# Optimization experiments

Measured on AMD Instinct MI355X. Metric: run time of the kernel, lower is better.

The kernel has to match this reference:

```python
import jax, jax.numpy as jnp
import numpy as np

B, F, C, H, W = 4, 16, 768, 16, 16   # video: b f c h w
L, M = 64, 16                        # audio: b c l m
NH = 12                              # num_heads
WS_V = 4                             # local_window (video window size, frames)
GROUPS = 32                          # GroupNorm32
EPS = 1e-5


def group_norm(x, scale, bias):
    # x: [b, c, t]; normalize over (channels-within-group, t)
    b, c, t = x.shape
    xg = x.reshape(b, GROUPS, c // GROUPS, t)
    mu = xg.mean(axis=(2, 3), keepdims=True)
    var = xg.var(axis=(2, 3), keepdims=True)
    xg = (xg - mu) * jax.lax.rsqrt(var + EPS)
    return xg.reshape(b, c, t) * scale[None, :, None] + bias[None, :, None]


def setup_inputs() -> dict:
    key = jax.random.key(0)
    ks = jax.random.split(key, 8)
    s = 0.02
    return {
        "video": jax.random.normal(ks[0], (B, F, C, H, W), jnp.float32),
        "audio": jax.random.normal(ks[1], (B, C, L, M), jnp.float32),
        "vn_scale": jnp.ones((C,), jnp.float32),
        "vn_bias": jnp.zeros((C,), jnp.float32),
        "an_scale": jnp.ones((C,), jnp.float32),
        "an_bias": jnp.zeros((C,), jnp.float32),
        "vqkv_w": jax.random.normal(ks[2], (3 * C, C), jnp.float32) * s,
        "vqkv_b": jnp.zeros((3 * C,), jnp.float32),
        "aqkv_w": jax.random.normal(ks[3], (3 * C, C), jnp.float32) * s,
        "aqkv_b": jnp.zeros((3 * C,), jnp.float32),
        "vproj_w": jax.random.normal(ks[4], (C, C), jnp.float32) * s,  # zero_module in orig; random for nontrivial baseline
        "vproj_b": jnp.zeros((C,), jnp.float32),
        "aproj_w": jax.random.normal(ks[5], (C, C), jnp.float32) * s,
        "aproj_b": jnp.zeros((C,), jnp.float32),
    }


def reference(video, audio, vn_scale, vn_bias, an_scale, an_bias,
              vqkv_w, vqkv_b, aqkv_w, aqkv_b,
              vproj_w, vproj_b, aproj_w, aproj_b):
    b, f, c, h, w = video.shape
    _, _, l, m = audio.shape
    ch = c // NH
    scale = ch ** -0.25
    ws_audio = WS_V * l // f
    nwin = f // WS_V
    wsv_tok = WS_V * h * w      # video tokens per window
    wsa_tok = ws_audio * m      # audio tokens per window

    vt = jnp.transpose(video, (0, 2, 1, 3, 4)).reshape(b, c, f * h * w)  # b c (f h w)
    at = audio.reshape(b, c, l * m)                                       # b c (l m)

    # 1x1 conv qkv after GroupNorm
    vqkv = jnp.einsum('oc,bct->bot', vqkv_w, group_norm(vt, vn_scale, vn_bias)) + vqkv_b[None, :, None]
    aqkv = jnp.einsum('oc,bct->bot', aqkv_w, group_norm(at, an_scale, an_bias)) + aqkv_b[None, :, None]
    q_v, k_v, v_v = jnp.split(vqkv, 3, axis=1)
    q_a, k_a, v_a = jnp.split(aqkv, 3, axis=1)

    # attention_index with window_shift = 0
    va_index = (jnp.arange(wsa_tok)[None, :] + (jnp.arange(nwin) * wsa_tok)[:, None]) % (l * m)
    av_index = (jnp.arange(wsv_tok)[None, :] + (jnp.arange(nwin) * wsv_tok)[:, None]) % (f * h * w)

    def heads(x):
        return x.reshape(b, NH, ch, -1)

    # video queries attend gathered audio windows
    qv = heads(q_v).reshape(b, NH, ch, nwin, wsv_tok)
    ka = jnp.take(heads(k_a), va_index, axis=-1)   # [b,NH,ch,nwin,wsa_tok]
    vav = jnp.take(heads(v_a), va_index, axis=-1)
    wts = jax.nn.softmax(jnp.einsum('bhcnt,bhcns->bhnts', qv * scale, ka * scale), axis=-1)
    v_out = jnp.einsum('bhnts,bhcns->bhcnt', wts, vav).reshape(b, c, f * h * w)

    # audio queries attend gathered video windows
    qa = heads(q_a).reshape(b, NH, ch, nwin, wsa_tok)
    kv = jnp.take(heads(k_v), av_index, axis=-1)   # [b,NH,ch,nwin,wsv_tok]
    vvv = jnp.take(heads(v_v), av_index, axis=-1)
    wts = jax.nn.softmax(jnp.einsum('bhcnt,bhcns->bhnts', qa * scale, kv * scale), axis=-1)
    a_out = jnp.einsum('bhnts,bhcns->bhcnt', wts, vvv).reshape(b, c, l * m)

    # zero-init 1x1x1 / 1x1 proj_out convs + residual
    vh = jnp.transpose(v_out.reshape(b, c, f, h, w), (0, 2, 1, 3, 4))  # b f c h w
    vh = jnp.einsum('oc,bfchw->bfohw', vproj_w, vh) + vproj_b[None, None, :, None, None]
    ah = jnp.einsum('oc,bclm->bolm', aproj_w, a_out.reshape(b, c, l, m)) + aproj_b[None, :, None, None]
    return video + vh, audio + ah
```

## Files before the change

kernel.cpp:

```cpp
#include <hip/hip_runtime.h>
#include <hip/hip_bf16.h>

typedef unsigned short ushort_t;
typedef __attribute__((ext_vector_type(8))) short short8;
typedef __attribute__((ext_vector_type(4))) float f32x4;

#define DI __device__ __forceinline__

DI float b2f(unsigned int u16) {
  union { unsigned int i; float f; } v;
  v.i = u16 << 16;
  return v.f;
}
DI ushort_t f2b(float f) {
  union { float f; unsigned int u; } v; v.f = f;
  unsigned int r = v.u + 0x7FFFu + ((v.u >> 16) & 1u);
  return (ushort_t)(r >> 16);
}

DI void gl_lds16(const ushort_t* g, ushort_t* l) {
  __builtin_amdgcn_global_load_lds(
      (const __attribute__((address_space(1))) unsigned int*)g,
      (__attribute__((address_space(3))) unsigned int*)l, 16, 0, 0);
}

__global__ void wcvt_kernel(const float* __restrict__ w0, const float* __restrict__ w1,
                            const float* __restrict__ w2, const float* __restrict__ w3,
                            ushort_t* __restrict__ o0, ushort_t* __restrict__ o1,
                            ushort_t* __restrict__ o2, ushort_t* __restrict__ o3) {
  const int n1 = 2304 * 768, n3 = 768 * 768;
  const int total = 2 * n1 + 2 * n3;
  for (int i = blockIdx.x * blockDim.x + threadIdx.x; i < total; i += gridDim.x * blockDim.x) {
    if (i < n1) o0[i] = f2b(w0[i]);
    else if (i < 2 * n1) o1[i - n1] = f2b(w1[i - n1]);
    else if (i < 2 * n1 + n3) o2[i - 2 * n1] = f2b(w2[i - 2 * n1]);
    else o3[i - 2 * n1 - n3] = f2b(w3[i - 2 * n1 - n3]);
  }
}

__global__ void gn_partial_kernel(const float* __restrict__ video,
                                  const float* __restrict__ audio,
                                  float* __restrict__ part) {
  const int bid = blockIdx.x;
  const int tid = threadIdx.x;
  float s = 0.f, ss = 0.f;
  if (bid < 2048) {
    int bg = bid >> 4, f = bid & 15;
    int b = bg >> 5, g = bg & 31;
    const float* base = video + ((size_t)((b * 16 + f) * 768 + g * 24)) * 256 + tid;
#pragma unroll
    for (int cl = 0; cl < 24; ++cl) {
      float v = base[cl * 256];
      s += v; ss += v * v;
    }
  } else {
    int a = bid - 2048;
    int bg = a >> 2, p = a & 3;
    int b = bg >> 5, g = bg & 31;
    const float* base = audio + ((size_t)(b * 768 + g * 24)) * 1024 + p * 256 + tid;
#pragma unroll
    for (int cl = 0; cl < 24; ++cl) {
      float v = base[cl * 1024];
      s += v; ss += v * v;
    }
  }
  for (int off = 32; off > 0; off >>= 1) { s += __shfl_down(s, off, 64); ss += __shfl_down(ss, off, 64); }
  __shared__ float red[8];
  int wv = tid >> 6, ln = tid & 63;
  if (ln == 0) { red[wv * 2] = s; red[wv * 2 + 1] = ss; }
  __syncthreads();
  if (tid == 0) {
    part[bid * 2] = red[0] + red[2] + red[4] + red[6];
    part[bid * 2 + 1] = red[1] + red[3] + red[5] + red[7];
  }
}

__global__ void gn_final_kernel(const float* __restrict__ part,
                                float* __restrict__ mu, float* __restrict__ rs) {
  const int tid = threadIdx.x;
  float s = 0.f, ss = 0.f;
  if (tid < 128) {
#pragma unroll
    for (int i = 0; i < 16; ++i) { s += part[(tid * 16 + i) * 2]; ss += part[(tid * 16 + i) * 2 + 1]; }
    const float N = 24.f * 4096.f;
    float m = s / N;
    mu[tid] = m;
    rs[tid] = rsqrtf(ss / N - m * m + 1e-5f);
  } else {
    int a = tid - 128;
#pragma unroll
    for (int i = 0; i < 4; ++i) { s += part[(2048 + a * 4 + i) * 2]; ss += part[(2048 + a * 4 + i) * 2 + 1]; }
    const float N = 24.f * 1024.f;
    float m = s / N;
    mu[tid] = m;
    rs[tid] = rsqrtf(ss / N - m * m + 1e-5f);
  }
}

__global__ void norm_video_kernel(const float* __restrict__ video,
                                  const float* __restrict__ mu, const float* __restrict__ rs,
                                  const float* __restrict__ sc, const float* __restrict__ bi,
                                  ushort_t* __restrict__ Xv) {
  __shared__ float T[32][257];
  const int bx = blockIdx.x;
  const int bf = bx / 24, ct = bx % 24;
  const int b = bf >> 4, f = bf & 15;
  const int c0 = ct * 32;
  const int tid = threadIdx.x;
  for (int i = 0; i < 32; ++i) {
    int c = c0 + i;
    int g = c / 24;
    float m = mu[b * 32 + g], r = rs[b * 32 + g];
    float v = video[((size_t)((b * 16 + f) * 768 + c)) * 256 + tid];
    T[i][tid] = (v - m) * r * sc[c] + bi[c];
  }
  __syncthreads();
  for (int i = 0; i < 32; ++i) {
    int id = i * 256 + tid;
    int c = id & 31, hw = id >> 5;
    Xv[((size_t)(b * 4096 + f * 256 + hw)) * 768 + c0 + c] = f2b(T[c][hw]);
  }
}

__global__ void norm_audio_kernel(const float* __restrict__ audio,
                                  const float* __restrict__ mu, const float* __restrict__ rs,
                                  const float* __restrict__ sc, const float* __restrict__ bi,
                                  ushort_t* __restrict__ Xa) {
  __shared__ float T[32][257];
  const int bx = blockIdx.x;
  const int bt = bx / 24, ct = bx % 24;
  const int b = bt >> 2, t0 = (bt & 3) * 256;
  const int c0 = ct * 32;
  const int tid = threadIdx.x;
  for (int i = 0; i < 32; ++i) {
    int c = c0 + i;
    int g = c / 24;
    float m = mu[128 + b * 32 + g], r = rs[128 + b * 32 + g];
    float v = audio[((size_t)(b * 768 + c)) * 1024 + t0 + tid];
    T[i][tid] = (v - m) * r * sc[c] + bi[c];
  }
  __syncthreads();
  for (int i = 0; i < 32; ++i) {
    int id = i * 256 + tid;
    int c = id & 31, tt = id >> 5;
    Xa[((size_t)(b * 1024 + t0 + tt)) * 768 + c0 + c] = f2b(T[c][tt]);
  }
}

template <int MODE>
__global__ __launch_bounds__(256) void gemm_kernel(
    const ushort_t* __restrict__ A, const ushort_t* __restrict__ W,
    const float* __restrict__ bias,
    void* __restrict__ p0, void* __restrict__ p1, void* __restrict__ p2,
    int M) {
  __shared__ ushort_t sm[32768];
  const int tid = threadIdx.x;
  const int lane = tid & 63, wave = tid >> 6;
  const int quad = lane >> 4, l16 = lane & 15;
  const int nwg = gridDim.x * gridDim.y;
  const int orig = blockIdx.x + gridDim.x * blockIdx.y;
  const int lid = (orig & 7) * (nwg >> 3) + (orig >> 3);
  const int n0 = (lid % gridDim.x) * 128, m0 = (lid / gridDim.x) * 128;
  const int wm = (wave & 1) * 64, wn = (wave >> 1) * 64;

  const int srow = wave * 32 + (lane >> 3);
  const int sq = ((lane & 7) ^ (lane >> 3)) * 8;
  const ushort_t* gA = A + (size_t)(m0 + srow) * 768 + sq;
  const ushort_t* gB = W + (size_t)(n0 + srow) * 768 + sq;

  f32x4 acc[4][4];
#pragma unroll
  for (int i = 0; i < 4; ++i)
#pragma unroll
    for (int j = 0; j < 4; ++j) acc[i][j] = (f32x4){0.f, 0.f, 0.f, 0.f};

  auto stage = [&](int kc, int cur) {
    ushort_t* lA = sm + cur * 8192 + wave * 2048;
    ushort_t* lB = sm + 16384 + cur * 8192 + wave * 2048;
#pragma unroll
    for (int i = 0; i < 4; ++i) {
      gl_lds16(gA + (size_t)i * 8 * 768 + kc, lA + i * 512);
      gl_lds16(gB + (size_t)i * 8 * 768 + kc, lB + i * 512);
    }
  };

  stage(0, 0);
  __syncthreads();
  int cur = 0;
  for (int t = 0; t < 12; ++t) {
    if (t < 11) stage((t + 1) * 64, cur ^ 1);
    const ushort_t* cA = sm + cur * 8192;
    const ushort_t* cB = sm + 16384 + cur * 8192;
#pragma unroll
    for (int ks = 0; ks < 2; ++ks) {
      short8 av[4], bv[4];
#pragma unroll
      for (int im = 0; im < 4; ++im) {
        int rr = wm + im * 16 + l16;
        av[im] = *reinterpret_cast<const short8*>(
            cA + rr * 64 + (((ks * 4 + quad) ^ (rr & 7)) * 8));
      }
#pragma unroll
      for (int in = 0; in < 4; ++in) {
        int rr = wn + in * 16 + l16;
        bv[in] = *reinterpret_cast<const short8*>(
            cB + rr * 64 + (((ks * 4 + quad) ^ (rr & 7)) * 8));
      }
#pragma unroll
      for (int im = 0; im < 4; ++im)
#pragma unroll
        for (int in = 0; in < 4; ++in)
          acc[im][in] = __builtin_amdgcn_mfma_f32_16x16x32_bf16(av[im], bv[in], acc[im][in], 0, 0, 0);
    }
    __syncthreads();
    cur ^= 1;
  }

  ushort_t* sC = sm;
  if (MODE == 0) {
    const int section = n0 / 768;
    const int obase = n0 - section * 768;
    if (section < 2) {
#pragma unroll
      for (int in = 0; in < 4; ++in) {
        int ol = wn + in * 16 + l16;
        float bv_ = bias[n0 + ol];
#pragma unroll
        for (int im = 0; im < 4; ++im)
#pragma unroll
          for (int r = 0; r < 4; ++r) {
            int row = wm + im * 16 + quad * 4 + r;
            sC[row * 136 + ol] = f2b(acc[im][in][r] + bv_);
          }
      }
      __syncthreads();
      ushort_t* dst = (ushort_t*)(section == 0 ? p0 : p1);
#pragma unroll
      for (int i = 0; i < 8; ++i) {
        int cid = i * 256 + tid;
        int row = cid >> 4, ch = cid & 15;
        *reinterpret_cast<uint4*>(dst + (size_t)(m0 + row) * 768 + obase + ch * 8) =
            *reinterpret_cast<const uint4*>(sC + row * 136 + ch * 8);
      }
    } else {
#pragma unroll
      for (int in = 0; in < 4; ++in) {
        int ol = wn + in * 16 + l16;
        float bv_ = bias[n0 + ol];
#pragma unroll
        for (int im = 0; im < 4; ++im)
#pragma unroll
          for (int r = 0; r < 4; ++r) {
            int mr = wm + im * 16 + quad * 4 + r;
            sC[ol * 136 + mr] = f2b(acc[im][in][r] + bv_);
          }
      }
      __syncthreads();
      ushort_t* dst = (ushort_t*)p2;
#pragma unroll
      for (int i = 0; i < 8; ++i) {
        int cid = i * 256 + tid;
        int o = cid >> 4, ch = cid & 15;
        *reinterpret_cast<uint4*>(dst + (size_t)(obase + o) * M + m0 + ch * 8) =
            *reinterpret_cast<const uint4*>(sC + o * 136 + ch * 8);
      }
    }
  } else {
#pragma unroll
    for (int in = 0; in < 4; ++in) {
      int ol = wn + in * 16 + l16;
      float bv_ = bias[n0 + ol];
#pragma unroll
      for (int im = 0; im < 4; ++im)
#pragma unroll
        for (int r = 0; r < 4; ++r) {
          int mr = wm + im * 16 + quad * 4 + r;
          sC[ol * 136 + mr] = f2b(acc[im][in][r] + bv_);
        }
    }
    __syncthreads();
    float* outp = (float*)p0;
    const float* resp = (const float*)p1;
#pragma unroll
    for (int i = 0; i < 16; ++i) {
      int cid = i * 256 + tid;
      int o = cid >> 5, ch = cid & 31;
      uint2 pk = *reinterpret_cast<const uint2*>(sC + o * 136 + ch * 4);
      size_t gidx;
      if (MODE == 1) {
        int b = m0 >> 12, f = (m0 >> 8) & 15, hw0 = m0 & 255;
        gidx = ((size_t)((b * 16 + f) * 768 + n0 + o)) * 256 + hw0 + ch * 4;
      } else {
        int b = m0 >> 10, t0 = m0 & 1023;
        gidx = ((size_t)(b * 768 + n0 + o)) * 1024 + t0 + ch * 4;
      }
      float4 rv = *reinterpret_cast<const float4*>(resp + gidx);
      float4 ov;
      ov.x = rv.x + b2f(pk.x & 0xffff);
      ov.y = rv.y + b2f(pk.x >> 16);
      ov.z = rv.z + b2f(pk.y & 0xffff);
      ov.w = rv.w + b2f(pk.y >> 16);
      *reinterpret_cast<float4*>(outp + gidx) = ov;
    }
  }
}

template <int QW, int SW>
__global__ __launch_bounds__(256) void attn_mfma_kernel(
    const ushort_t* __restrict__ Qt, const ushort_t* __restrict__ Kt,
    const ushort_t* __restrict__ Vc, ushort_t* __restrict__ Ot,
    int TQb, int TSb, int Ms) {
  __shared__ ushort_t sK[128 * 72];
  __shared__ ushort_t sP[64 * 136];
  const int tid = threadIdx.x;
  const int lane = tid & 63, wave = tid >> 6;
  const int quad = lane >> 4, l16 = lane & 15;
  const int NQT = QW / 64;
  const int bx = blockIdx.x;
  const int qt = bx % NQT;
  const int win = (bx / NQT) & 3;
  const int h = (bx / (NQT * 4)) % 12;
  const int b = bx / (NQT * 48);
  const int hc = h * 64;
  const int nq0 = b * TQb + win * QW + qt * 64;
  const int ns_base = b * TSb + win * SW;

#pragma unroll
  for (int i = 0; i < 2; ++i) {
    int c = i * 256 + tid;
    int row = c >> 3, cc = c & 7;
    uint4 raw = *reinterpret_cast<const uint4*>(Qt + (size_t)(nq0 + row) * 768 + hc + cc * 8);
    unsigned int* rp = reinterpret_cast<unsigned int*>(&raw);
    uint4 out;
    unsigned int* op = reinterpret_cast<unsigned int*>(&out);
#pragma unroll
    for (int j = 0; j < 4; ++j) {
      unsigned int lo = (unsigned int)f2b(0.125f * b2f(rp[j] & 0xffff));
      unsigned int hi = (unsigned int)f2b(0.125f * b2f(rp[j] >> 16));
      op[j] = lo | (hi << 16);
    }
    *reinterpret_cast<uint4*>(sK + row * 72 + cc * 8) = out;
  }
  __syncthreads();
  short8 qf[2];
#pragma unroll
  for (int ks = 0; ks < 2; ++ks)
    qf[ks] = *reinterpret_cast<const short8*>(sK + (wave * 16 + l16) * 72 + ks * 32 + quad * 8);

  float mr[4], lr[4];
  f32x4 on[4];
#pragma unroll
  for (int r = 0; r < 4; ++r) { mr[r] = -1e30f; lr[r] = 0.f; }
#pragma unroll
  for (int nc = 0; nc < 4; ++nc) on[nc] = (f32x4){0.f, 0.f, 0.f, 0.f};

  for (int t = 0; t < SW / 128; ++t) {
    const int ns0 = ns_base + t * 128;
    __syncthreads();
#pragma unroll
    for (int i = 0; i < 4; ++i) {
      int c = i * 256 + tid;
      int row = c >> 3, cc = c & 7;
      *reinterpret_cast<uint4*>(sK + row * 72 + cc * 8) =
          *reinterpret_cast<const uint4*>(Kt + (size_t)(ns0 + row) * 768 + hc + cc * 8);
    }
    __syncthreads();
    f32x4 sf[8];
#pragma unroll
    for (int nt = 0; nt < 8; ++nt) sf[nt] = (f32x4){0.f, 0.f, 0.f, 0.f};
#pragma unroll
    for (int ks = 0; ks < 2; ++ks) {
#pragma unroll
      for (int nt = 0; nt < 8; ++nt) {
        short8 kf = *reinterpret_cast<const short8*>(sK + (nt * 16 + l16) * 72 + ks * 32 + quad * 8);
        sf[nt] = __builtin_amdgcn_mfma_f32_16x16x32_bf16(qf[ks], kf, sf[nt], 0, 0, 0);
      }
    }
#pragma unroll
    for (int r = 0; r < 4; ++r) {
      float m_ = sf[0][r];
#pragma unroll
      for (int nt = 1; nt < 8; ++nt) m_ = fmaxf(m_, sf[nt][r]);
#pragma unroll
      for (int off = 1; off < 16; off <<= 1) m_ = fmaxf(m_, __shfl_xor(m_, off));
      float mnew = fmaxf(mr[r], m_);
      float al = __expf(mr[r] - mnew);
      float ls = 0.f;
      int prow = (wave * 16 + quad * 4 + r) * 136;
#pragma unroll
      for (int nt = 0; nt < 8; ++nt) {
        float p = __expf(sf[nt][r] - mnew);
        ls += p;
        sP[prow + nt * 16 + l16] = f2b(p);
      }
#pragma unroll
      for (int off = 1; off < 16; off <<= 1) ls += __shfl_xor(ls, off);
      lr[r] = lr[r] * al + ls;
      mr[r] = mnew;
#pragma unroll
      for (int nc = 0; nc < 4; ++nc) on[nc][r] *= al;
    }
    __syncthreads();
#pragma unroll
    for (int i = 0; i < 4; ++i) {
      int c = i * 256 + tid;
      int ch = c >> 4, cc = c & 15;
      *reinterpret_cast<uint4*>(sK + ch * 136 + cc * 8) =
          *reinterpret_cast<const uint4*>(Vc + (size_t)(hc + ch) * Ms + ns0 + cc * 8);
    }
    __syncthreads();
#pragma unroll
    for (int ks = 0; ks < 4; ++ks) {
      short8 pf = *reinterpret_cast<const short8*>(sP + (wave * 16 + l16) * 136 + ks * 32 + quad * 8);
#pragma unroll
      for (int nc = 0; nc < 4; ++nc) {
        short8 vf = *reinterpret_cast<const short8*>(sK + (nc * 16 + l16) * 136 + ks * 32 + quad * 8);
        on[nc] = __builtin_amdgcn_mfma_f32_16x16x32_bf16(pf, vf, on[nc], 0, 0, 0);
      }
    }
  }
#pragma unroll
  for (int r = 0; r < 4; ++r) {
    float inv = 1.f / lr[r];
    int prow = (wave * 16 + quad * 4 + r) * 136;
#pragma unroll
    for (int nc = 0; nc < 4; ++nc)
      sP[prow + nc * 16 + l16] = f2b(on[nc][r] * inv);
  }
  __syncthreads();
#pragma unroll
  for (int i = 0; i < 2; ++i) {
    int c = i * 256 + tid;
    int row = c >> 3, cc = c & 7;
    *reinterpret_cast<uint4*>(Ot + (size_t)(nq0 + row) * 768 + hc + cc * 8) =
        *reinterpret_cast<const uint4*>(sP + row * 136 + cc * 8);
  }
}

extern "C" void kernel_launch(void* const* d_in, const int* in_sizes, int n_in,
                              void* d_out, int out_size, void* d_ws, size_t ws_size,
                              hipStream_t stream) {
  (void)in_sizes; (void)n_in; (void)out_size; (void)ws_size;
  const float* video = (const float*)d_in[0];
  const float* audio = (const float*)d_in[1];
  const float* vn_s = (const float*)d_in[2];
  const float* vn_b = (const float*)d_in[3];
  const float* an_s = (const float*)d_in[4];
  const float* an_b = (const float*)d_in[5];
  const float* vqkv_w = (const float*)d_in[6];
  const float* vqkv_b = (const float*)d_in[7];
  const float* aqkv_w = (const float*)d_in[8];
  const float* aqkv_b = (const float*)d_in[9];
  const float* vproj_w = (const float*)d_in[10];
  const float* vproj_b = (const float*)d_in[11];
  const float* aproj_w = (const float*)d_in[12];
  const float* aproj_b = (const float*)d_in[13];

  float* out_v = (float*)d_out;
  float* out_a = out_v + (size_t)4 * 16 * 768 * 16 * 16;

  char* ws = (char*)d_ws;
  size_t off = 0;
  auto carve = [&](size_t bytes) {
    char* p = ws + off;
    off += (bytes + 255) & ~(size_t)255;
    return p;
  };
  float* mu = (float*)carve(256 * 4);
  float* rs = (float*)carve(256 * 4);
  float* part = (float*)carve(2560 * 2 * 4);
  ushort_t* Xv = (ushort_t*)carve((size_t)16384 * 768 * 2);
  ushort_t* Xa = (ushort_t*)carve((size_t)4096 * 768 * 2);
  ushort_t* Wqv = (ushort_t*)carve((size_t)2304 * 768 * 2);
  ushort_t* Wqa = (ushort_t*)carve((size_t)2304 * 768 * 2);
  ushort_t* Wpv = (ushort_t*)carve((size_t)768 * 768 * 2);
  ushort_t* Wpa = (ushort_t*)carve((size_t)768 * 768 * 2);
  ushort_t* Qv = (ushort_t*)carve((size_t)16384 * 768 * 2);
  ushort_t* Kv = (ushort_t*)carve((size_t)16384 * 768 * 2);
  ushort_t* Vv = (ushort_t*)carve((size_t)16384 * 768 * 2);
  ushort_t* Qa = (ushort_t*)carve((size_t)4096 * 768 * 2);
  ushort_t* Ka = (ushort_t*)carve((size_t)4096 * 768 * 2);
  ushort_t* Va = (ushort_t*)carve((size_t)4096 * 768 * 2);
  ushort_t* Ov = Xv;
  ushort_t* Oa = Xa;

  wcvt_kernel<<<1024, 256, 0, stream>>>(vqkv_w, aqkv_w, vproj_w, aproj_w, Wqv, Wqa, Wpv, Wpa);
  gn_partial_kernel<<<2560, 256, 0, stream>>>(video, audio, part);
  gn_final_kernel<<<1, 256, 0, stream>>>(part, mu, rs);
  norm_video_kernel<<<1536, 256, 0, stream>>>(video, mu, rs, vn_s, vn_b, Xv);
  norm_audio_kernel<<<384, 256, 0, stream>>>(audio, mu, rs, an_s, an_b, Xa);
  gemm_kernel<0><<<dim3(18, 128), 256, 0, stream>>>(Xv, Wqv, vqkv_b, Qv, Kv, Vv, 16384);
  gemm_kernel<0><<<dim3(18, 32), 256, 0, stream>>>(Xa, Wqa, aqkv_b, Qa, Ka, Va, 4096);
  attn_mfma_kernel<1024, 256><<<3072, 256, 0, stream>>>(Qv, Ka, Va, Ov, 4096, 1024, 4096);
  attn_mfma_kernel<256, 1024><<<768, 256, 0, stream>>>(Qa, Kv, Vv, Oa, 1024, 4096, 16384);
  gemm_kernel<1><<<dim3(6, 128), 256, 0, stream>>>(Ov, Wpv, vproj_b, (void*)out_v, (void*)video, nullptr, 16384);
  gemm_kernel<2><<<dim3(6, 32), 256, 0, stream>>>(Oa, Wpa, aproj_b, (void*)out_a, (void*)audio, nullptr, 4096);
}
```

Before: 400.3 us.

## Pipeline attention K/V staging with async LDS loads and fold q scaling into GEMM

Rewrites the windowed attention kernel to stage Q, K and V with direct global-to-LDS loads into XOR-swizzled unpadded tiles. V is double-buffered and the next K tile is prefetched after the QK^T MFMAs, so loads overlap compute. This cuts the per-tile barriers from four to about two. The 0.125 query scale moves into the QKV GEMM epilogue for the q section, which removes the per-block bf16 unpack, rescale and repack. LDS use grows to about 73KB per block, which may lower occupancy.

After: 403.1 us. No clear change (+0.7%).

```diff
diff --git a/kernel.cpp b/kernel.cpp
--- a/kernel.cpp
+++ b/kernel.cpp
@@ -221,6 +221,7 @@
     const int section = n0 / 768;
     const int obase = n0 - section * 768;
     if (section < 2) {
+      const float qs = (section == 0) ? 0.125f : 1.0f;
 #pragma unroll
       for (int in = 0; in < 4; ++in) {
         int ol = wn + in * 16 + l16;
@@ -230,7 +231,7 @@
 #pragma unroll
           for (int r = 0; r < 4; ++r) {
             int row = wm + im * 16 + quad * 4 + r;
-            sC[row * 136 + ol] = f2b(acc[im][in][r] + bv_);
+            sC[row * 136 + ol] = f2b((acc[im][in][r] + bv_) * qs);
           }
       }
       __syncthreads();
@@ -310,12 +311,17 @@
     const ushort_t* __restrict__ Qt, const ushort_t* __restrict__ Kt,
     const ushort_t* __restrict__ Vc, ushort_t* __restrict__ Ot,
     int TQb, int TSb, int Ms) {
-  __shared__ ushort_t sK[128 * 72];
-  __shared__ ushort_t sP[64 * 136];
+  __shared__ ushort_t sm[37376];
+  ushort_t* sQ = sm;
+  ushort_t* sK = sm + 4096;
+  ushort_t* sV0 = sm + 12288;
+  ushort_t* sV1 = sm + 20480;
+  ushort_t* sP = sm + 28672;
   const int tid = threadIdx.x;
   const int lane = tid & 63, wave = tid >> 6;
   const int quad = lane >> 4, l16 = lane & 15;
   const int NQT = QW / 64;
+  const int NT = SW / 128;
   const int bx = blockIdx.x;
   const int qt = bx % NQT;
   const int win = (bx / NQT) & 3;
@@ -325,27 +331,40 @@
   const int nq0 = b * TQb + win * QW + qt * 64;
   const int ns_base = b * TSb + win * SW;
 
+  const int r8 = lane >> 3, c8 = lane & 7;
+  const int s8 = (c8 ^ r8) * 8;
+  const int r16 = lane >> 4, c16 = lane & 15;
+
+  auto stage_k = [&](int ns0) {
+#pragma unroll
+    for (int i = 0; i < 4; ++i) {
+      int row = wave * 32 + i * 8 + r8;
+      gl_lds16(Kt + (size_t)(ns0 + row) * 768 + hc + s8, sK + (wave * 32 + i * 8) * 64);
+    }
+  };
+  auto stage_v = [&](int ns0, ushort_t* sV) {
+#pragma unroll
+    for (int i = 0; i < 4; ++i) {
+      int ch = wave * 16 + i * 4 + r16;
+      int slot = c16 ^ (i * 4 + r16);
+      gl_lds16(Vc + (size_t)(hc + ch) * Ms + ns0 + slot * 8, sV + (wave * 16 + i * 4) * 128);
+    }
+  };
+
 #pragma unroll
   for (int i = 0; i < 2; ++i) {
-    int c = i * 256 + tid;
-    int row = c >> 3, cc = c & 7;
-    uint4 raw = *reinterpret_cast<const uint4*>(Qt + (size_t)(nq0 + row) * 768 + hc + cc * 8);
-    unsigned int* rp = reinterpret_cast<unsigned int*>(&raw);
-    uint4 out;
-    unsigned int* op = reinterpret_cast<unsigned int*>(&out);
-#pragma unroll
-    for (int j = 0; j < 4; ++j) {
-      unsigned int lo = (unsigned int)f2b(0.125f * b2f(rp[j] & 0xffff));
-      unsigned int hi = (unsigned int)f2b(0.125f * b2f(rp[j] >> 16));
-      op[j] = lo | (hi << 16);
-    }
-    *reinterpret_cast<uint4*>(sK + row * 72 + cc * 8) = out;
-  }
+    int row = wave * 16 + i * 8 + r8;
+    gl_lds16(Qt + (size_t)(nq0 + row) * 768 + hc + s8, sQ + (wave * 16 + i * 8) * 64);
+  }
+  stage_k(ns_base);
+  stage_v(ns_base, sV0);
   __syncthreads();
+
   short8 qf[2];
 #pragma unroll
   for (int ks = 0; ks < 2; ++ks)
-    qf[ks] = *reinterpret_cast<const short8*>(sK + (wave * 16 + l16) * 72 + ks * 32 + quad * 8);
+    qf[ks] = *reinterpret_cast<const short8*>(
+        sQ + (wave * 16 + l16) * 64 + (((ks * 4 + quad) ^ (l16 & 7)) * 8));
 
   float mr[4], lr[4];
   f32x4 on[4];
@@ -354,28 +373,22 @@
 #pragma unroll
   for (int nc = 0; nc < 4; ++nc) on[nc] = (f32x4){0.f, 0.f, 0.f, 0.f};
 
-  for (int t = 0; t < SW / 128; ++t) {
-    const int ns0 = ns_base + t * 128;
+  for (int t = 0; t < NT; ++t) {
+    if (t + 1 < NT) stage_v(ns_base + (t + 1) * 128, (t & 1) ? sV0 : sV1);
+    f32x4 sf[8];
+#pragma unroll
+    for (int nt = 0; nt < 8; ++nt) sf[nt] = (f32x4){0.f, 0.f, 0.f, 0.f};
+#pragma unroll
+    for (int ks = 0; ks < 2; ++ks) {
+#pragma unroll
+      for (int nt = 0; nt < 8; ++nt) {
+        short8 kf = *reinterpret_cast<const short8*>(
+            sK + (nt * 16 + l16) * 64 + (((ks * 4 + quad) ^ (l16 & 7)) * 8));
+        sf[nt] = __builtin_amdgcn_mfma_f32_16x16x32_bf16(qf[ks], kf, sf[nt], 0, 0, 0);
+      }
+    }
     __syncthreads();
-#pragma unroll
-    for (int i = 0; i < 4; ++i) {
-      int c = i * 256 + tid;
-      int row = c >> 3, cc = c & 7;
-      *reinterpret_cast<uint4*>(sK + row * 72 + cc * 8) =
-          *reinterpret_cast<const uint4*>(Kt + (size_t)(ns0 + row) * 768 + hc + cc * 8);
-    }
-    __syncthreads();
-    f32x4 sf[8];
-#pragma unroll
-    for (int nt = 0; nt < 8; ++nt) sf[nt] = (f32x4){0.f, 0.f, 0.f, 0.f};
-#pragma unroll
-    for (int ks = 0; ks < 2; ++ks) {
-#pragma unroll
-      for (int nt = 0; nt < 8; ++nt) {
-        short8 kf = *reinterpret_cast<const short8*>(sK + (nt * 16 + l16) * 72 + ks * 32 + quad * 8);
-        sf[nt] = __builtin_amdgcn_mfma_f32_16x16x32_bf16(qf[ks], kf, sf[nt], 0, 0, 0);
-      }
-    }
+    if (t + 1 < NT) stage_k(ns_base + (t + 1) * 128);
 #pragma unroll
     for (int r = 0; r < 4; ++r) {
       float m_ = sf[0][r];
@@ -400,24 +413,18 @@
 #pragma unroll
       for (int nc = 0; nc < 4; ++nc) on[nc][r] *= al;
     }
-    __syncthreads();
-#pragma unroll
-    for (int i = 0; i < 4; ++i) {
-      int c = i * 256 + tid;
-      int ch = c >> 4, cc = c & 15;
-      *reinterpret_cast<uint4*>(sK + ch * 136 + cc * 8) =
-          *reinterpret_cast<const uint4*>(Vc + (size_t)(hc + ch) * Ms + ns0 + cc * 8);
-    }
-    __syncthreads();
+    const ushort_t* sV = (t & 1) ? sV1 : sV0;
 #pragma unroll
     for (int ks = 0; ks < 4; ++ks) {
       short8 pf = *reinterpret_cast<const short8*>(sP + (wave * 16 + l16) * 136 + ks * 32 + quad * 8);
 #pragma unroll
       for (int nc = 0; nc < 4; ++nc) {
-        short8 vf = *reinterpret_cast<const short8*>(sK + (nc * 16 + l16) * 136 + ks * 32 + quad * 8);
+        short8 vf = *reinterpret_cast<const short8*>(
+            sV + (nc * 16 + l16) * 128 + (((ks * 4 + quad) ^ l16) * 8));
         on[nc] = __builtin_amdgcn_mfma_f32_16x16x32_bf16(pf, vf, on[nc], 0, 0, 0);
       }
     }
+    if (t + 1 < NT) __syncthreads();
   }
 #pragma unroll
   for (int r = 0; r < 4; ++r) {
```
